# Kernel tuning notes

Measured on AMD Instinct MI355X. Metric: run time of the kernel, lower is better.

The kernel has to match this reference:

```python
import jax, jax.numpy as jnp
import numpy as np
import math

NUM_HEADS = 32
NUM_KV_HEADS = 8
HEAD_DIM = 128
HIDDEN = 4096
BATCH = 2
SEQ = 2048
MASK_MIN = -1e9


def _rope(x, cos, sin):
    # x: [B, S, H, D], cos/sin: [S, D/2]
    d2 = x.shape[-1] // 2
    x1, x2 = x[..., :d2], x[..., d2:]
    c = cos[None, :, None, :]
    s = sin[None, :, None, :]
    return jnp.concatenate([x1 * c - x2 * s, x2 * c + x1 * s], axis=-1)


def setup_inputs() -> dict:
    key = jax.random.key(0)
    k1, k2, k3 = jax.random.split(key, 3)
    hidden_states = jax.random.normal(k1, (BATCH, SEQ, HIDDEN), dtype=jnp.float32) * 0.02
    Wqkv = jax.random.normal(k2, (HIDDEN, (NUM_HEADS + 2 * NUM_KV_HEADS) * HEAD_DIM), dtype=jnp.float32) * (HIDDEN ** -0.5)
    Wo = jax.random.normal(k3, (NUM_HEADS * HEAD_DIM, HIDDEN), dtype=jnp.float32) * (HIDDEN ** -0.5)
    pos = np.arange(SEQ, dtype=np.float32)
    inv_freq = 1.0 / (10000.0 ** (np.arange(0, HEAD_DIM, 2, dtype=np.float32) / HEAD_DIM))
    freqs = np.outer(pos, inv_freq)  # [S, D/2]
    cos = jnp.asarray(np.cos(freqs), dtype=jnp.float32)
    sin = jnp.asarray(np.sin(freqs), dtype=jnp.float32)
    # causal additive mask [B, 1, S, S]
    causal = np.triu(np.full((SEQ, SEQ), MASK_MIN, dtype=np.float32), k=1)
    attention_mask = jnp.broadcast_to(jnp.asarray(causal)[None, None], (BATCH, 1, SEQ, SEQ))
    return {"hidden_states": hidden_states, "Wqkv": Wqkv, "Wo": Wo,
            "cos": cos, "sin": sin, "attention_mask": attention_mask}


def reference(hidden_states, Wqkv, Wo, cos, sin, attention_mask):
    B, S, H = hidden_states.shape
    n_rep = NUM_HEADS // NUM_KV_HEADS
    qkv = jnp.einsum('bsh,hd->bsd', hidden_states, Wqkv)
    q_end = NUM_HEADS * HEAD_DIM
    k_end = q_end + NUM_KV_HEADS * HEAD_DIM
    q = qkv[..., :q_end].reshape(B, S, NUM_HEADS, HEAD_DIM)
    k = qkv[..., q_end:k_end].reshape(B, S, NUM_KV_HEADS, HEAD_DIM)
    v = qkv[..., k_end:].reshape(B, S, NUM_KV_HEADS, HEAD_DIM)
    q = _rope(q, cos, sin)
    k = _rope(k, cos, sin)
    # repeat_kv: expand kv heads to query heads
    k = jnp.repeat(k, n_rep, axis=2)  # [B, S, NH, D]
    v = jnp.repeat(v, n_rep, axis=2)
    scores = jnp.einsum('bqhd,bkhd->bhqk', q, k) / math.sqrt(HEAD_DIM)
    scores = scores + attention_mask
    scores = jnp.maximum(scores, jnp.finfo(scores.dtype).min)
    probs = jax.nn.softmax(scores.astype(jnp.float32), axis=-1).astype(q.dtype)
    attn = jnp.einsum('bhqk,bkhd->bqhd', probs, v)  # [B, S, NH, D]
    attn = attn.reshape(B, S, NUM_HEADS * HEAD_DIM)
    return jnp.einsum('bsd,dh->bsh', attn, Wo)
```

## Files before the change

kernel.cpp:

```cpp
#include <hip/hip_runtime.h>

typedef unsigned short u16;
typedef __bf16 bf16x8 __attribute__((ext_vector_type(8)));
typedef float f32x4 __attribute__((ext_vector_type(4)));
typedef float f32x16 __attribute__((ext_vector_type(16)));
typedef u16 u16x4 __attribute__((ext_vector_type(4)));

#define SEQ 2048
#define NQKV 6144
#define HID 4096

__device__ inline u16 f2bf(float f) {
  union { float f; unsigned u; } x; x.f = f;
  unsigned r = x.u + 0x7fffu + ((x.u >> 16) & 1u);
  return (u16)(r >> 16);
}
__device__ inline float bf2f(u16 u) {
  union { unsigned u; float f; } x; x.u = ((unsigned)u) << 16;
  return x.f;
}
__device__ inline f32x4 mfma16(bf16x8 a, bf16x8 b, f32x4 c) {
  return __builtin_amdgcn_mfma_f32_16x16x32_bf16(a, b, c, 0, 0, 0);
}
__device__ inline f32x16 mfma32(bf16x8 a, bf16x8 b, f32x16 c) {
  return __builtin_amdgcn_mfma_f32_32x32x16_bf16(a, b, c, 0, 0, 0);
}
__device__ inline unsigned cvtpk(float lo, float hi) {
  unsigned r;
  asm("v_cvt_pk_bf16_f32 %0, %1, %2" : "=v"(r) : "v"(lo), "v"(hi));
  return r;
}
__device__ inline void gload16(const void* g, void* l) {
  __builtin_amdgcn_global_load_lds((const __attribute__((address_space(1))) void*)g,
                                   (__attribute__((address_space(3))) void*)l,
                                   16, 0, 0);
}

__global__ __launch_bounds__(256) void conv_kernel(const float* __restrict__ in,
                                                   u16* __restrict__ out) {
  int i = (blockIdx.x * 256 + threadIdx.x) * 4;
  float4 v = *(const float4*)(in + i);
  u16x4 o;
  o[0] = f2bf(v.x); o[1] = f2bf(v.y); o[2] = f2bf(v.z); o[3] = f2bf(v.w);
  *(u16x4*)(out + i) = o;
}

__global__ __launch_bounds__(256) void transconv_kernel(const float* __restrict__ in,
                                                        u16* __restrict__ out,
                                                        int R, int C) {
  __shared__ u16 tile[32][33];
  int c0 = blockIdx.x * 32, r0 = blockIdx.y * 32;
  int tx = threadIdx.x & 31, ty = threadIdx.x >> 5;
  for (int i = 0; i < 4; ++i)
    tile[ty + 8 * i][tx] = f2bf(in[(size_t)(r0 + ty + 8 * i) * C + c0 + tx]);
  __syncthreads();
  for (int i = 0; i < 4; ++i)
    out[(size_t)(c0 + ty + 8 * i) * R + r0 + tx] = tile[tx][ty + 8 * i];
}

__device__ inline void store_out(u16* p, float v) { *p = f2bf(v); }
__device__ inline void store_out(float* p, float v) { *p = v; }

template <typename OutT>
__global__ __launch_bounds__(512, 2) void gemm_kernel(const u16* __restrict__ A,
                                                      const u16* __restrict__ Bt,
                                                      OutT* __restrict__ C,
                                                      int M, int N, int K, int nby) {
  __shared__ __align__(16) u16 As[2][2][256 * 32];
  __shared__ __align__(16) u16 Bs[2][2][256 * 32];
  int nwg = gridDim.x;
  int bid = blockIdx.x;
  int s = (bid & 7) * (nwg >> 3) + (bid >> 3);
  int by = s % nby, bx = s / nby;
  int row0 = by * 256, col0 = bx * 256;
  int tid = threadIdx.x, w = tid >> 6, l = tid & 63;
  int wm = w >> 2, wn = w & 3;
  int lo = l & 15, hi = l >> 4;
  int sr = tid >> 2;
  int sc = tid & 3;
  int lc = sc ^ ((tid >> 3) & 3);
  const u16* Ab = A + (size_t)row0 * K;
  const u16* Bb = Bt + (size_t)col0 * K;
  int nkt = K >> 6;

  f32x4 acc[8][4] = {};

#define STA(tt, kh)                                                           \
  { _Pragma("unroll")                                                         \
    for (int j = 0; j < 2; ++j) {                                             \
      int row = j * 128 + sr;                                                 \
      gload16(Ab + (size_t)row * K + (tt) * 64 + (kh) * 32 + lc * 8,          \
              &As[(tt) & 1][kh][row * 32 + sc * 8]);                          \
    } }
#define STB(tt, kh)                                                           \
  { _Pragma("unroll")                                                         \
    for (int j = 0; j < 2; ++j) {                                             \
      int row = j * 128 + sr;                                                 \
      gload16(Bb + (size_t)row * K + (tt) * 64 + (kh) * 32 + lc * 8,          \
              &Bs[(tt) & 1][kh][row * 32 + sc * 8]);                          \
    } }
#define RA(cur, kh, fm, dst)                                                  \
  { int r = wm * 128 + (fm) * 16 + lo;                                        \
    dst = *(const bf16x8*)&As[cur][kh][r * 32 + ((hi ^ ((r >> 1) & 3)) * 8)]; }
#define RB(cur, kh, fn, dst)                                                  \
  { int r = wn * 64 + (fn) * 16 + lo;                                         \
    dst = *(const bf16x8*)&Bs[cur][kh][r * 32 + ((hi ^ ((r >> 1) & 3)) * 8)]; }

  STA(0, 0); STB(0, 0); STA(0, 1); STB(0, 1);
  asm volatile("s_waitcnt vmcnt(4)" ::: "memory");
  __builtin_amdgcn_s_barrier();

  bf16x8 af[4], bfr[4];
  for (int t = 0; t < nkt; ++t) {
    int cur = t & 1;
    bool pf = (t + 1 < nkt);
    RA(cur, 0, 0, af[0]); RA(cur, 0, 1, af[1]); RA(cur, 0, 2, af[2]); RA(cur, 0, 3, af[3]);
    RB(cur, 0, 0, bfr[0]); RB(cur, 0, 1, bfr[1]); RB(cur, 0, 2, bfr[2]); RB(cur, 0, 3, bfr[3]);
    if (pf) STA(t + 1, 0);
    __builtin_amdgcn_s_barrier();
    asm volatile("s_waitcnt lgkmcnt(0)" ::: "memory");
    __builtin_amdgcn_s_setprio(1);
#pragma unroll
    for (int fm = 0; fm < 4; ++fm)
#pragma unroll
      for (int fn = 0; fn < 4; ++fn)
        acc[fm][fn] = mfma16(af[fm], bfr[fn], acc[fm][fn]);
    __builtin_amdgcn_s_setprio(0);
    __builtin_amdgcn_s_barrier();
    RA(cur, 0, 4, af[0]); RA(cur, 0, 5, af[1]); RA(cur, 0, 6, af[2]); RA(cur, 0, 7, af[3]);
    if (pf) STB(t + 1, 0);
    __builtin_amdgcn_s_barrier();
    asm volatile("s_waitcnt lgkmcnt(0)" ::: "memory");
    __builtin_amdgcn_s_setprio(1);
#pragma unroll
    for (int fm = 0; fm < 4; ++fm)
#pragma unroll
      for (int fn = 0; fn < 4; ++fn)
        acc[4 + fm][fn] = mfma16(af[fm], bfr[fn], acc[4 + fm][fn]);
    __builtin_amdgcn_s_setprio(0);
    if (pf) { asm volatile("s_waitcnt vmcnt(4)" ::: "memory"); }
    else    { asm volatile("s_waitcnt vmcnt(0)" ::: "memory"); }
    __builtin_amdgcn_s_barrier();
    RA(cur, 1, 0, af[0]); RA(cur, 1, 1, af[1]); RA(cur, 1, 2, af[2]); RA(cur, 1, 3, af[3]);
    RB(cur, 1, 0, bfr[0]); RB(cur, 1, 1, bfr[1]); RB(cur, 1, 2, bfr[2]); RB(cur, 1, 3, bfr[3]);
    if (pf) STA(t + 1, 1);
    __builtin_amdgcn_s_barrier();
    asm volatile("s_waitcnt lgkmcnt(0)" ::: "memory");
    __builtin_amdgcn_s_setprio(1);
#pragma unroll
    for (int fm = 0; fm < 4; ++fm)
#pragma unroll
      for (int fn = 0; fn < 4; ++fn)
        acc[fm][fn] = mfma16(af[fm], bfr[fn], acc[fm][fn]);
    __builtin_amdgcn_s_setprio(0);
    __builtin_amdgcn_s_barrier();
    RA(cur, 1, 4, af[0]); RA(cur, 1, 5, af[1]); RA(cur, 1, 6, af[2]); RA(cur, 1, 7, af[3]);
    if (pf) STB(t + 1, 1);
    __builtin_amdgcn_s_barrier();
    asm volatile("s_waitcnt lgkmcnt(0)" ::: "memory");
    __builtin_amdgcn_s_setprio(1);
#pragma unroll
    for (int fm = 0; fm < 4; ++fm)
#pragma unroll
      for (int fn = 0; fn < 4; ++fn)
        acc[4 + fm][fn] = mfma16(af[fm], bfr[fn], acc[4 + fm][fn]);
    __builtin_amdgcn_s_setprio(0);
    if (pf) { asm volatile("s_waitcnt vmcnt(4)" ::: "memory"); }
    __builtin_amdgcn_s_barrier();
  }
#undef STA
#undef STB
#undef RA
#undef RB

  for (int fm = 0; fm < 8; ++fm)
    for (int fn = 0; fn < 4; ++fn)
      for (int rr = 0; rr < 4; ++rr) {
        int row = row0 + wm * 128 + fm * 16 + hi * 4 + rr;
        int col = col0 + wn * 64 + fn * 16 + lo;
        store_out(&C[(size_t)row * N + col], acc[fm][fn][rr]);
      }
}

__global__ __launch_bounds__(256) void rope_kernel(u16* __restrict__ qkv,
                                                   const float* __restrict__ cosb,
                                                   const float* __restrict__ sinb) {
  int idx = blockIdx.x * 256 + threadIdx.x;
  int d = idx & 63;
  int head = (idx >> 6) % 40;
  int m = idx / (64 * 40);
  int s = m & (SEQ - 1);
  int col = head < 32 ? head * 128 : 4096 + (head - 32) * 128;
  u16* p = qkv + (size_t)m * NQKV + col;
  float x1 = bf2f(p[d]), x2 = bf2f(p[d + 64]);
  float c = cosb[s * 64 + d], sn = sinb[s * 64 + d];
  p[d] = f2bf(x1 * c - x2 * sn);
  p[d + 64] = f2bf(x2 * c + x1 * sn);
}

__global__ __launch_bounds__(256) void vtrans_kernel(const u16* __restrict__ qkv,
                                                     u16* __restrict__ Vt) {
  __shared__ u16 tile[32][33];
  int bid = blockIdx.x;
  int dt = bid & 3;
  int st = (bid >> 2) & 63;
  int bk = bid >> 8;
  int b = bk >> 3, kvh = bk & 7;
  int tx = threadIdx.x & 31, ty = threadIdx.x >> 5;
  for (int i = 0; i < 4; ++i) {
    int s = st * 32 + ty + 8 * i;
    tile[ty + 8 * i][tx] = qkv[(size_t)(b * SEQ + s) * NQKV + 5120 + kvh * 128 + dt * 32 + tx];
  }
  __syncthreads();
  for (int i = 0; i < 4; ++i) {
    int d = dt * 32 + ty + 8 * i;
    Vt[((size_t)bk * 128 + d) * SEQ + st * 32 + tx] = tile[tx][ty + 8 * i];
  }
}

__global__ __launch_bounds__(256, 2) void flash_kernel(const u16* __restrict__ qkv,
                                                       const u16* __restrict__ Vt,
                                                       u16* __restrict__ attn) {
  const float C2 = 0.12751740f;
  int bid = blockIdx.x;
  int bh = bid & 63;
  int pr = bid >> 6;
  int h = bh & 31;
  int b = bh >> 5;
  int w = threadIdx.x >> 6, l = threadIdx.x & 63;
  int hv = l >> 5;
  int q32 = l & 31;
  int kvh = h >> 2;

  __shared__ __align__(16) u16 Ks[2][64 * 128];
  __shared__ __align__(16) u16 Vs[2][128 * 64];

  const u16* kb = qkv + (size_t)(b * SEQ) * NQKV + 4096 + kvh * 128;
  const u16* vtb = Vt + (size_t)(b * 8 + kvh) * 128 * SEQ;

#define STAGEKV(TT, BF)                                                       \
  { _Pragma("unroll")                                                         \
    for (int i = 0; i < 4; ++i) {                                             \
      int ck = w * 4 + i;                                                     \
      int rk = ck * 4 + (l >> 4);                                             \
      gload16(kb + (size_t)((TT) * 64 + rk) * NQKV + (((l & 15) ^ (rk & 7)) * 8), \
              &Ks[BF][ck * 512]);                                             \
      int rv = ck * 8 + (l >> 3);                                             \
      gload16(vtb + (size_t)rv * SEQ + (TT) * 64 + (((l & 7) ^ (rv & 7)) * 8), \
              &Vs[BF][ck * 512]);                                             \
    } }

  for (int pass = 0; pass < 2; ++pass) {
    int qc = pass ? 15 - pr : pr;
    int q0 = qc * 128 + w * 32;
    int qg = q0 + q32;
    __syncthreads();

    bf16x8 qf[8];
    {
      const u16* qr = qkv + (size_t)(b * SEQ + qg) * NQKV + h * 128 + hv * 8;
#pragma unroll
      for (int d0 = 0; d0 < 8; ++d0) qf[d0] = *(const bf16x8*)(qr + d0 * 16);
    }
    f32x16 o[4] = {};
    float mreg = -1e30f, lreg = 0.f;
    int ktend = 2 * qc + 1;
    int mykt = 2 * qc + (w >> 1);

    STAGEKV(0, 0);
    for (int kt = 0; kt <= ktend; ++kt) {
      int buf = kt & 1;
      if (kt < ktend) {
        STAGEKV(kt + 1, buf ^ 1);
        asm volatile("s_waitcnt vmcnt(8)" ::: "memory");
      } else {
        asm volatile("s_waitcnt vmcnt(0)" ::: "memory");
      }
      __builtin_amdgcn_s_barrier();

      if (kt <= mykt) {
        f32x16 s0 = {}, s1 = {};
        int swzk = q32 & 7;
#pragma unroll
        for (int d0 = 0; d0 < 8; ++d0) {
          int sl = (((d0 * 2 + hv) ^ swzk) * 8);
          bf16x8 k0 = *(const bf16x8*)&Ks[buf][q32 * 128 + sl];
          bf16x8 k1 = *(const bf16x8*)&Ks[buf][(32 + q32) * 128 + sl];
          s0 = mfma32(k0, qf[d0], s0);
          s1 = mfma32(k1, qf[d0], s1);
        }
        if (kt == mykt) {
#pragma unroll
          for (int r = 0; r < 16; ++r) {
            int kloc = (r & 3) + 8 * (r >> 2) + 4 * hv;
            if (kt * 64 + kloc > qg) s0[r] = -1e30f;
            if (kt * 64 + 32 + kloc > qg) s1[r] = -1e30f;
          }
        }
        float pm = -1e30f;
#pragma unroll
        for (int r = 0; r < 16; ++r) {
          pm = fmaxf(pm, s0[r]);
          pm = fmaxf(pm, s1[r]);
        }
        pm = fmaxf(pm, __shfl_xor(pm, 32));
        if (!__all(pm - mreg <= 62.746f)) {
          float mnew = fmaxf(mreg, pm);
          float al = exp2f((mreg - mnew) * C2);
          lreg *= al;
#pragma unroll
          for (int r = 0; r < 16; ++r) {
            o[0][r] *= al; o[1][r] *= al; o[2][r] *= al; o[3][r] *= al;
          }
          mreg = mnew;
        }
        float rs = 0.f;
#pragma unroll
        for (int r = 0; r < 16; ++r) {
          s0[r] = exp2f((s0[r] - mreg) * C2); rs += s0[r];
          s1[r] = exp2f((s1[r] - mreg) * C2); rs += s1[r];
        }
        rs += __shfl_xor(rs, 32);
        lreg += rs;
        bf16x8 pa[4];
#define MKPA(KSI, SP, RB)                                                     \
        { unsigned wA = cvtpk(SP[(RB) + 0], SP[(RB) + 1]);                    \
          unsigned wB = cvtpk(SP[(RB) + 2], SP[(RB) + 3]);                    \
          unsigned wC = cvtpk(SP[(RB) + 4], SP[(RB) + 5]);                    \
          unsigned wD = cvtpk(SP[(RB) + 6], SP[(RB) + 7]);                    \
          unsigned sA = __shfl_xor(wA, 32), sB = __shfl_xor(wB, 32);          \
          unsigned sC = __shfl_xor(wC, 32), sD = __shfl_xor(wD, 32);          \
          union { unsigned u[4]; bf16x8 v; } pk;                              \
          pk.u[0] = hv ? sC : wA; pk.u[1] = hv ? sD : wB;                     \
          pk.u[2] = hv ? wC : sA; pk.u[3] = hv ? wD : sB;                     \
          pa[KSI] = pk.v; }
        MKPA(0, s0, 0) MKPA(1, s0, 8) MKPA(2, s1, 0) MKPA(3, s1, 8)
#undef MKPA
#pragma unroll
        for (int db = 0; db < 4; ++db) {
          int rv = db * 32 + q32;
          int swz = rv & 7;
#pragma unroll
          for (int ks = 0; ks < 4; ++ks) {
            bf16x8 vf = *(const bf16x8*)&Vs[buf][rv * 64 + (((ks * 2 + hv) ^ swz) * 8)];
            o[db] = mfma32(vf, pa[ks], o[db]);
          }
        }
      }
    }
    float invl = 1.0f / lreg;
    u16* op = attn + (size_t)(b * SEQ + qg) * 4096 + h * 128 + hv * 4;
#pragma unroll
    for (int db = 0; db < 4; ++db)
#pragma unroll
      for (int g = 0; g < 4; ++g) {
        unsigned w0 = cvtpk(o[db][g * 4 + 0] * invl, o[db][g * 4 + 1] * invl);
        unsigned w1 = cvtpk(o[db][g * 4 + 2] * invl, o[db][g * 4 + 3] * invl);
        uint2 val; val.x = w0; val.y = w1;
        *(uint2*)(op + db * 32 + g * 8) = val;
      }
  }
#undef STAGEKV
}

extern "C" void kernel_launch(void* const* d_in, const int* in_sizes, int n_in,
                              void* d_out, int out_size, void* d_ws, size_t ws_size,
                              hipStream_t stream) {
  const float* hidden = (const float*)d_in[0];
  const float* Wqkv = (const float*)d_in[1];
  const float* Wo = (const float*)d_in[2];
  const float* cosb = (const float*)d_in[3];
  const float* sinb = (const float*)d_in[4];
  float* out = (float*)d_out;

  char* ws = (char*)d_ws;
  u16* R1 = (u16*)ws;
  u16* R2 = (u16*)(ws + 50331648);
  u16* R3 = (u16*)(ws + 100663296);

  conv_kernel<<<16384, 256, 0, stream>>>(hidden, R3);
  transconv_kernel<<<dim3(6144 / 32, 4096 / 32), 256, 0, stream>>>(Wqkv, R1, 4096, 6144);
  gemm_kernel<u16><<<384, 512, 0, stream>>>(R3, R1, R2, 4096, 6144, 4096, 16);
  rope_kernel<<<40960, 256, 0, stream>>>(R2, cosb, sinb);
  vtrans_kernel<<<4096, 256, 0, stream>>>(R2, R3);
  flash_kernel<<<512, 256, 0, stream>>>(R2, R3, R1);
  transconv_kernel<<<dim3(4096 / 32, 4096 / 32), 256, 0, stream>>>(Wo, R2, 4096, 4096);
  gemm_kernel<float><<<256, 512, 0, stream>>>(R1, R2, out, 4096, 4096, 4096, 16);
}
```

Before: 553.2 us.

## Use 256x384 tile GEMM with 32x32 MFMA and triple buffering for QKV projection

Adds a new GEMM kernel for the QKV projection that uses 256x384 output tiles, 32x32x16 bf16 MFMA instructions and a three-stage LDS ring with prefetch two K-steps ahead. The grid becomes 256 workgroups, which matches the CU count, instead of 384 workgroups with 256x256 tiles. The aim is more reuse per LDS load, fewer scheduling waves and better overlap of loads with compute. The cost is a large accumulator footprint of 192 floats per thread, which risks register pressure at two workgroups per CU. Output stores are scalar bf16 writes.

New measurement: 518.2 us (median of 3 runs). 1.07x faster.

```diff
diff --git a/kernel.cpp b/kernel.cpp
--- a/kernel.cpp
+++ b/kernel.cpp
@@ -56,6 +56,111 @@
   __syncthreads();
   for (int i = 0; i < 4; ++i)
     out[(size_t)(c0 + ty + 8 * i) * R + r0 + tx] = tile[tx][ty + 8 * i];
+}
+
+__global__ __launch_bounds__(512, 2) void gemm32_kernel(const u16* __restrict__ A,
+                                                        const u16* __restrict__ Bt,
+                                                        u16* __restrict__ C,
+                                                        int M, int N, int K, int nby) {
+  __shared__ __align__(16) u16 As[3][256 * 32];
+  __shared__ __align__(16) u16 Bs[3][384 * 32];
+  int nwg = gridDim.x;
+  int bid = blockIdx.x;
+  int s = (bid & 7) * (nwg >> 3) + (bid >> 3);
+  int by = s % nby, bx = s / nby;
+  int row0 = by * 256, col0 = bx * 384;
+  int tid = threadIdx.x, w = tid >> 6, l = tid & 63;
+  int wm = w >> 2, wn = w & 3;
+  int l31 = l & 31, lh = l >> 5;
+  const u16* Ab = A + (size_t)row0 * K;
+  const u16* Bb = Bt + (size_t)col0 * K;
+  int nkt = K >> 5;
+
+  f32x16 acc[4][3] = {};
+
+#define STA32(tt, bf)                                                         \
+  { _Pragma("unroll")                                                         \
+    for (int j = 0; j < 2; ++j) {                                             \
+      int cid = j * 512 + tid;                                                \
+      int row = cid >> 2, cl = cid & 3;                                       \
+      gload16(Ab + (size_t)row * K + (tt) * 32 + ((cl ^ ((row >> 1) & 3)) * 8), \
+              &As[bf][cid * 8]);                                              \
+    } }
+#define STB32(tt, bf)                                                         \
+  { _Pragma("unroll")                                                         \
+    for (int j = 0; j < 3; ++j) {                                             \
+      int cid = j * 512 + tid;                                                \
+      int row = cid >> 2, cl = cid & 3;                                       \
+      gload16(Bb + (size_t)row * K + (tt) * 32 + ((cl ^ ((row >> 1) & 3)) * 8), \
+              &Bs[bf][cid * 8]);                                              \
+    } }
+#define RA32(bf, im, ks, dst)                                                 \
+  { int r = wm * 128 + (im) * 32 + l31;                                       \
+    dst = *(const bf16x8*)&As[bf][r * 32 + ((((ks) * 2 + lh) ^ ((r >> 1) & 3)) * 8)]; }
+#define RB32(bf, in, ks, dst)                                                 \
+  { int r = wn * 96 + (in) * 32 + l31;                                        \
+    dst = *(const bf16x8*)&Bs[bf][r * 32 + ((((ks) * 2 + lh) ^ ((r >> 1) & 3)) * 8)]; }
+
+  STA32(0, 0); STB32(0, 0); STA32(1, 1); STB32(1, 1);
+  asm volatile("s_waitcnt vmcnt(5)" ::: "memory");
+  __builtin_amdgcn_s_barrier();
+
+  int cur = 0;
+  for (int t = 0; t < nkt; ++t) {
+    int nb = cur + 2; if (nb >= 3) nb -= 3;
+    bool pf = (t + 2 < nkt);
+    bf16x8 a0, a1, a2, a3, b0, b1, b2;
+    RA32(cur, 0, 0, a0); RA32(cur, 1, 0, a1); RA32(cur, 2, 0, a2); RA32(cur, 3, 0, a3);
+    RB32(cur, 0, 0, b0); RB32(cur, 1, 0, b1); RB32(cur, 2, 0, b2);
+    if (pf) STA32(t + 2, nb);
+    __builtin_amdgcn_s_barrier();
+    asm volatile("s_waitcnt lgkmcnt(0)" ::: "memory");
+    __builtin_amdgcn_s_setprio(1);
+    acc[0][0] = mfma32(a0, b0, acc[0][0]); acc[0][1] = mfma32(a0, b1, acc[0][1]);
+    acc[0][2] = mfma32(a0, b2, acc[0][2]);
+    acc[1][0] = mfma32(a1, b0, acc[1][0]); acc[1][1] = mfma32(a1, b1, acc[1][1]);
+    acc[1][2] = mfma32(a1, b2, acc[1][2]);
+    acc[2][0] = mfma32(a2, b0, acc[2][0]); acc[2][1] = mfma32(a2, b1, acc[2][1]);
+    acc[2][2] = mfma32(a2, b2, acc[2][2]);
+    acc[3][0] = mfma32(a3, b0, acc[3][0]); acc[3][1] = mfma32(a3, b1, acc[3][1]);
+    acc[3][2] = mfma32(a3, b2, acc[3][2]);
+    __builtin_amdgcn_s_setprio(0);
+    __builtin_amdgcn_s_barrier();
+    RA32(cur, 0, 1, a0); RA32(cur, 1, 1, a1); RA32(cur, 2, 1, a2); RA32(cur, 3, 1, a3);
+    RB32(cur, 0, 1, b0); RB32(cur, 1, 1, b1); RB32(cur, 2, 1, b2);
+    if (pf) STB32(t + 2, nb);
+    __builtin_amdgcn_s_barrier();
+    asm volatile("s_waitcnt lgkmcnt(0)" ::: "memory");
+    __builtin_amdgcn_s_setprio(1);
+    acc[0][0] = mfma32(a0, b0, acc[0][0]); acc[0][1] = mfma32(a0, b1, acc[0][1]);
+    acc[0][2] = mfma32(a0, b2, acc[0][2]);
+    acc[1][0] = mfma32(a1, b0, acc[1][0]); acc[1][1] = mfma32(a1, b1, acc[1][1]);
+    acc[1][2] = mfma32(a1, b2, acc[1][2]);
+    acc[2][0] = mfma32(a2, b0, acc[2][0]); acc[2][1] = mfma32(a2, b1, acc[2][1]);
+    acc[2][2] = mfma32(a2, b2, acc[2][2]);
+    acc[3][0] = mfma32(a3, b0, acc[3][0]); acc[3][1] = mfma32(a3, b1, acc[3][1]);
+    acc[3][2] = mfma32(a3, b2, acc[3][2]);
+    __builtin_amdgcn_s_setprio(0);
+    if (pf)              { asm volatile("s_waitcnt vmcnt(5)" ::: "memory"); }
+    else if (t + 1 < nkt){ asm volatile("s_waitcnt vmcnt(0)" ::: "memory"); }
+    __builtin_amdgcn_s_barrier();
+    cur = cur + 1 == 3 ? 0 : cur + 1;
+  }
+#undef STA32
+#undef STB32
+#undef RA32
+#undef RB32
+
+#pragma unroll
+  for (int im = 0; im < 4; ++im)
+#pragma unroll
+    for (int in = 0; in < 3; ++in)
+#pragma unroll
+      for (int reg = 0; reg < 16; ++reg) {
+        int row = row0 + wm * 128 + im * 32 + (reg & 3) + 8 * (reg >> 2) + 4 * lh;
+        int col = col0 + wn * 96 + in * 32 + l31;
+        C[(size_t)row * N + col] = f2bf(acc[im][in][reg]);
+      }
 }
 
 __device__ inline void store_out(u16* p, float v) { *p = f2bf(v); }
@@ -380,7 +485,7 @@
 
   conv_kernel<<<16384, 256, 0, stream>>>(hidden, R3);
   transconv_kernel<<<dim3(6144 / 32, 4096 / 32), 256, 0, stream>>>(Wqkv, R1, 4096, 6144);
-  gemm_kernel<u16><<<384, 512, 0, stream>>>(R3, R1, R2, 4096, 6144, 4096, 16);
+  gemm32_kernel<<<256, 512, 0, stream>>>(R3, R1, R2, 4096, 6144, 4096, 16);
   rope_kernel<<<40960, 256, 0, stream>>>(R2, cosb, sinb);
   vtrans_kernel<<<4096, 256, 0, stream>>>(R2, R3);
   flash_kernel<<<512, 256, 0, stream>>>(R2, R3, R1);
```
